# Performance work log

Hardware: AMD Instinct MI355X
Metric: run time of the kernel (lower is better)

## Reference

```python
import math
import jax, jax.numpy as jnp
import numpy as np

N_HEADS = 16
D_KV = 64
NUM_BUCKETS = 32
MAX_DISTANCE = 128


def _relative_position_bucket(relative_position, num_buckets=NUM_BUCKETS, max_distance=MAX_DISTANCE):
    # bidirectional=True (encoder)
    num_buckets //= 2
    n = -relative_position
    ret = (n < 0).astype(jnp.int32) * num_buckets
    n = jnp.abs(n)
    max_exact = num_buckets // 2
    is_small = n < max_exact
    val_if_large = max_exact + (
        jnp.log(jnp.maximum(n, 1).astype(jnp.float32) / max_exact)
        / math.log(max_distance / max_exact)
        * (num_buckets - max_exact)
    ).astype(jnp.int32)
    val_if_large = jnp.minimum(val_if_large, num_buckets - 1)
    return ret + jnp.where(is_small, n, val_if_large)


def setup_inputs() -> dict:
    key = jax.random.key(0)
    ks = jax.random.split(key, 6)
    B, S, D = 2, 2048, 1024
    scale = 0.02  # keep pre-softmax logits in a sane range
    return {
        "x": jax.random.normal(ks[0], (B, S, D), dtype=jnp.float32),
        "Wq": jax.random.normal(ks[1], (D, N_HEADS * D_KV), dtype=jnp.float32) * scale,
        "Wk": jax.random.normal(ks[2], (D, N_HEADS * D_KV), dtype=jnp.float32) * scale,
        "Wv": jax.random.normal(ks[3], (D, N_HEADS * D_KV), dtype=jnp.float32) * scale,
        "Wo": jax.random.normal(ks[4], (N_HEADS * D_KV, D), dtype=jnp.float32) * scale,
        "rel_emb": jax.random.normal(ks[5], (NUM_BUCKETS, N_HEADS), dtype=jnp.float32) * scale,
    }


def reference(x, Wq, Wk, Wv, Wo, rel_emb):
    B, S, D = x.shape
    H, Dk = N_HEADS, D_KV

    def shape(t):  # [B,S,H*Dk] -> [B,H,S,Dk]
        return t.reshape(B, S, H, Dk).transpose(0, 2, 1, 3)

    q = shape(x @ Wq)
    k = shape(x @ Wk)
    v = shape(x @ Wv)

    # NOTE: T5 attention has NO 1/sqrt(d) scaling.
    scores = jnp.einsum("bhqd,bhkd->bhqk", q, k)

    # relative position bias: [1, H, S, S]
    ctx_pos = jnp.arange(S)[:, None]
    mem_pos = jnp.arange(S)[None, :]
    rp_bucket = _relative_position_bucket(mem_pos - ctx_pos)  # [S, S]
    position_bias = rel_emb[rp_bucket].transpose(2, 0, 1)[None]  # [1,H,S,S]

    weights = jax.nn.softmax(scores + position_bias, axis=-1)
    context = jnp.einsum("bhqk,bhkd->bhqd", weights, v)
    context = context.transpose(0, 2, 1, 3).reshape(B, S, H * Dk)
    return context @ Wo
```

## Files before the change

kernel.cpp:

```cpp
#include <hip/hip_runtime.h>
#include <math.h>

typedef unsigned short u16;
typedef unsigned int u32;
typedef __attribute__((ext_vector_type(8))) short bf16x8_t;
typedef __attribute__((ext_vector_type(4))) float f32x4_t;

#define S_LEN  2048
#define NH     16
#define DK     64
#define DMODEL 1024
#define MROWS  4096

__device__ inline u16 f2b(float f) {
  union { float f; u32 u; } c; c.f = f;
  u32 u = c.u;
  return (u16)((u + 0x7fffu + ((u >> 16) & 1u)) >> 16);
}

__global__ void prep_kernel(const float* __restrict__ x,
                            const float* __restrict__ Wq, const float* __restrict__ Wk,
                            const float* __restrict__ Wv, const float* __restrict__ Wo,
                            const float* __restrict__ rel,
                            u16* __restrict__ xb, u16* __restrict__ Wall,
                            u16* __restrict__ Wto, float* __restrict__ btab) {
  __shared__ float tile[32][33];
  const int bid = blockIdx.x, t = threadIdx.x;
  if (bid < 4096) {
    int i = (bid * 256 + t) * 4;
    float4 v = *(const float4*)(x + i);
    ushort4 o;
    o.x = f2b(v.x); o.y = f2b(v.y); o.z = f2b(v.z); o.w = f2b(v.w);
    *(ushort4*)(xb + i) = o;
  } else if (bid < 8192) {
    int bid2 = bid - 4096;
    int z = bid2 >> 10, rem = bid2 & 1023;
    const float* W; u16* Wt;
    switch (z) {
      case 0: W = Wq; Wt = Wall; break;
      case 1: W = Wk; Wt = Wall + (size_t)DMODEL * DMODEL; break;
      case 2: W = Wv; Wt = Wall + (size_t)2 * DMODEL * DMODEL; break;
      default: W = Wo; Wt = Wto; break;
    }
    int bc = (rem & 31) * 32, br = (rem >> 5) * 32;
    int tx = t & 31, ty = t >> 5;
    #pragma unroll
    for (int yy = 0; yy < 32; yy += 8)
      tile[ty + yy][tx] = W[(size_t)(br + ty + yy) * DMODEL + bc + tx];
    __syncthreads();
    #pragma unroll
    for (int yy = 0; yy < 32; yy += 8)
      Wt[(size_t)(bc + ty + yy) * DMODEL + br + tx] = f2b(tile[tx][ty + yy]);
  } else {
    int idx = (bid - 8192) * 256 + t;
    if (idx < NH * 4095) {
      int h = idx / 4095;
      int dpos = idx - h * 4095;
      int delta = dpos - 2047;
      int ret = (delta > 0) ? 16 : 0;
      int n = delta < 0 ? -delta : delta;
      int bucket;
      if (n < 8) {
        bucket = ret + n;
      } else {
        float vf = logf((float)n * 0.125f) / 2.7725887222397811f * 8.0f;
        int vil = 8 + (int)vf;
        bucket = ret + (vil < 15 ? vil : 15);
      }
      btab[idx] = rel[bucket * NH + h] - 16.0f;
    }
  }
}

#define GSTR 56
__global__ __launch_bounds__(256) void gemm128_kernel(const u16* __restrict__ A,
                                                      const u16* __restrict__ Bt,
                                                      float* __restrict__ C,
                                                      u16* __restrict__ q16,
                                                      u16* __restrict__ k16,
                                                      u16* __restrict__ vt16,
                                                      int mode) {
  __shared__ __align__(16) u16 As[128 * GSTR];
  __shared__ __align__(16) u16 Bs[128 * GSTR];
  const int t = threadIdx.x, w = t >> 6, l = t & 63;
  const int c = l & 15, quad = l >> 4;
  const int m0 = blockIdx.x * 128, n0 = blockIdx.y * 128;
  const int wm = (w & 1) * 64, wn = (w >> 1) * 64;

  const int sr = t >> 2;
  const int k8 = (t & 3) * 8;
  const u16* Ag0 = A  + (size_t)(m0 + sr) * DMODEL + k8;
  const u16* Ag1 = Ag0 + (size_t)64 * DMODEL;
  const u16* Bg0 = Bt + (size_t)(n0 + sr) * DMODEL + k8;
  const u16* Bg1 = Bg0 + (size_t)64 * DMODEL;
  u16* Al0 = As + sr * GSTR + k8;
  u16* Al1 = Al0 + 64 * GSTR;
  u16* Bl0 = Bs + sr * GSTR + k8;
  u16* Bl1 = Bl0 + 64 * GSTR;

  uint4 a0 = *(const uint4*)Ag0, a1 = *(const uint4*)Ag1;
  uint4 b0 = *(const uint4*)Bg0, b1 = *(const uint4*)Bg1;

  f32x4_t acc[16] = {};
  for (int k0 = 0; k0 < DMODEL; k0 += 32) {
    __syncthreads();
    *(uint4*)Al0 = a0; *(uint4*)Al1 = a1;
    *(uint4*)Bl0 = b0; *(uint4*)Bl1 = b1;
    __syncthreads();
    if (k0 + 32 < DMODEL) {
      a0 = *(const uint4*)(Ag0 + k0 + 32);
      a1 = *(const uint4*)(Ag1 + k0 + 32);
      b0 = *(const uint4*)(Bg0 + k0 + 32);
      b1 = *(const uint4*)(Bg1 + k0 + 32);
    }
    bf16x8_t af[4], bfr[4];
    #pragma unroll
    for (int i = 0; i < 4; ++i) {
      af[i]  = *(const bf16x8_t*)(As + (wm + i * 16 + c) * GSTR + quad * 8);
      bfr[i] = *(const bf16x8_t*)(Bs + (wn + i * 16 + c) * GSTR + quad * 8);
    }
    #pragma unroll
    for (int mt = 0; mt < 4; ++mt)
      #pragma unroll
      for (int nt = 0; nt < 4; ++nt)
        acc[mt * 4 + nt] = __builtin_amdgcn_mfma_f32_16x16x32_bf16(af[mt], bfr[nt], acc[mt * 4 + nt], 0, 0, 0);
  }

  const int whichblk = n0 >> 10;
  if (mode == 0) {
    #pragma unroll
    for (int mt = 0; mt < 4; ++mt) {
      int grow0 = m0 + wm + mt * 16 + quad * 4;
      #pragma unroll
      for (int nt = 0; nt < 4; ++nt) {
        int gcol = n0 + wn + nt * 16 + c;
        #pragma unroll
        for (int r = 0; r < 4; ++r)
          C[(size_t)(grow0 + r) * DMODEL + gcol] = acc[mt * 4 + nt][r];
      }
    }
  } else if (whichblk == 2) {
    #pragma unroll
    for (int mt = 0; mt < 4; ++mt) {
      int grow0 = m0 + wm + mt * 16 + quad * 4;
      int b = grow0 >> 11, s0 = grow0 & 2047;
      #pragma unroll
      for (int nt = 0; nt < 4; ++nt) {
        int cc = (n0 + wn + nt * 16 + c) & 1023;
        int hh = cc >> 6, dk = cc & 63;
        f32x4_t v4 = acc[mt * 4 + nt];
        ushort4 o;
        o.x = f2b(v4[0]); o.y = f2b(v4[1]); o.z = f2b(v4[2]); o.w = f2b(v4[3]);
        *(ushort4*)(vt16 + (((size_t)(b * NH + hh)) * DK + dk) * S_LEN + s0) = o;
      }
    }
  } else {
    u16* tb = (w & 1) ? Bs : As;
    const int base_mw = m0 + wm;
    const int bb = base_mw >> 11, s0g = base_mw & 2047;
    const int cc = (n0 + wn) & 1023;
    const int hh = cc >> 6;
    u16* qk = (whichblk == 0 ? q16 : k16) + (((size_t)(bb * NH + hh)) * S_LEN + s0g) * DK;
    __syncthreads();
    #pragma unroll
    for (int round = 0; round < 2; ++round) {
      if ((w >> 1) == round) {
        #pragma unroll
        for (int mt = 0; mt < 4; ++mt)
          #pragma unroll
          for (int nt = 0; nt < 4; ++nt)
            #pragma unroll
            for (int r = 0; r < 4; ++r)
              tb[(mt * 16 + quad * 4 + r) * 72 + nt * 16 + c] = f2b(acc[mt * 4 + nt][r]);
        #pragma unroll
        for (int i = 0; i < 8; ++i) {
          int lrow = i * 8 + (l >> 3);
          int chk = l & 7;
          uint4 vv = *(const uint4*)(tb + lrow * 72 + chk * 8);
          *(uint4*)(qk + (size_t)lrow * DK + chk * 8) = vv;
        }
      }
      __syncthreads();
    }
  }
}

#define ASTR 72
__global__ __launch_bounds__(256, 4) void attn_mfma_kernel(const u16* __restrict__ q,
                                                           const u16* __restrict__ k,
                                                           const u16* __restrict__ vt,
                                                           const float* __restrict__ btab,
                                                           u16* __restrict__ ctx) {
  __shared__ __align__(16) u16 Ks[64 * ASTR];
  __shared__ __align__(16) u16 Vts[64 * ASTR];
  __shared__ __align__(16) u16 Ps[4 * 16 * ASTR];
  __shared__ float band[128];

  const int t = threadIdx.x;
  const int w = t >> 6, l = t & 63;
  const int c = l & 15, quad = l >> 4;
  const int bh = blockIdx.y;
  const int h = bh & (NH - 1), b = bh >> 4;
  const int q0 = blockIdx.x * 64;

  const u16* qb = q + (size_t)bh * S_LEN * DK;
  const u16* kb = k + (size_t)bh * S_LEN * DK;
  const u16* vb = vt + (size_t)bh * DK * S_LEN;
  const float* btp = btab + h * 4095 + (2047 - 63 - q0);

  bf16x8_t qfrag[2];
  {
    const u16* qp = qb + (size_t)(q0 + w * 16 + c) * DK + quad * 8;
    qfrag[0] = *(const bf16x8_t*)(qp);
    qfrag[1] = *(const bf16x8_t*)(qp + 32);
  }

  float lp[4] = {0.f, 0.f, 0.f, 0.f};
  f32x4_t O[4] = {};

  const int srow = t >> 3;
  const int sc8 = (t & 7) * 8;
  const u16* kg0 = kb + (size_t)srow * DK + sc8;
  const u16* kg1 = kg0 + (size_t)32 * DK;
  const u16* vg0 = vb + (size_t)srow * S_LEN + sc8;
  const u16* vg1 = vg0 + (size_t)32 * S_LEN;
  u16* Kl0 = Ks + srow * ASTR + sc8;
  u16* Kl1 = Kl0 + 32 * ASTR;
  u16* Vl0 = Vts + srow * ASTR + sc8;
  u16* Vl1 = Vl0 + 32 * ASTR;
  u16* Pw = Ps + w * 16 * ASTR;
  const int bnd0 = c - (w * 16 + quad * 4) + 63;

  uint4 kr0 = *(const uint4*)kg0, kr1 = *(const uint4*)kg1;
  uint4 vr0 = *(const uint4*)vg0, vr1 = *(const uint4*)vg1;
  float br = (t < 127) ? btp[t] : 0.f;

  for (int kt = 0; kt < S_LEN; kt += 64) {
    const int D = kt - q0;
    const bool far = (D >= 192) || (D <= -192);
    *(uint4*)Kl0 = kr0; *(uint4*)Kl1 = kr1;
    *(uint4*)Vl0 = vr0; *(uint4*)Vl1 = vr1;
    if (t < 127) band[t] = br;
    __syncthreads();
    if (kt + 64 < S_LEN) {
      kr0 = *(const uint4*)(kg0 + (size_t)(kt + 64) * DK);
      kr1 = *(const uint4*)(kg1 + (size_t)(kt + 64) * DK);
      vr0 = *(const uint4*)(vg0 + (kt + 64));
      vr1 = *(const uint4*)(vg1 + (kt + 64));
      br = (t < 127) ? btp[kt + 64 + t] : 0.f;
    }

    f32x4_t s4[4] = {};
    #pragma unroll
    for (int kc = 0; kc < 2; ++kc) {
      #pragma unroll
      for (int nt = 0; nt < 4; ++nt) {
        bf16x8_t bfr = *(const bf16x8_t*)(Ks + (nt * 16 + c) * ASTR + kc * 32 + quad * 8);
        s4[nt] = __builtin_amdgcn_mfma_f32_16x16x32_bf16(qfrag[kc], bfr, s4[nt], 0, 0, 0);
      }
    }

    if (far) {
      const float bf = btp[kt + 63];
      #pragma unroll
      for (int nt = 0; nt < 4; ++nt) {
        #pragma unroll
        for (int r = 0; r < 4; ++r) {
          float p = __expf(s4[nt][r] + bf);
          lp[r] += p;
          union { float f; u32 u; } cv; cv.f = p;
          Pw[(quad * 4 + r) * ASTR + nt * 16 + c] = (u16)((cv.u + 0x8000u) >> 16);
        }
      }
    } else {
      #pragma unroll
      for (int nt = 0; nt < 4; ++nt) {
        #pragma unroll
        for (int r = 0; r < 4; ++r) {
          float p = __expf(s4[nt][r] + band[bnd0 + nt * 16 - r]);
          lp[r] += p;
          union { float f; u32 u; } cv; cv.f = p;
          Pw[(quad * 4 + r) * ASTR + nt * 16 + c] = (u16)((cv.u + 0x8000u) >> 16);
        }
      }
    }

    #pragma unroll
    for (int kc = 0; kc < 2; ++kc) {
      bf16x8_t afr = *(const bf16x8_t*)(Pw + c * ASTR + kc * 32 + quad * 8);
      #pragma unroll
      for (int nt = 0; nt < 4; ++nt) {
        bf16x8_t bfr = *(const bf16x8_t*)(Vts + (nt * 16 + c) * ASTR + kc * 32 + quad * 8);
        O[nt] = __builtin_amdgcn_mfma_f32_16x16x32_bf16(afr, bfr, O[nt], 0, 0, 0);
      }
    }
    __syncthreads();
  }

  #pragma unroll
  for (int off = 1; off < 16; off <<= 1)
    #pragma unroll
    for (int r = 0; r < 4; ++r)
      lp[r] += __shfl_xor(lp[r], off, 64);
  #pragma unroll
  for (int r = 0; r < 4; ++r) {
    float inv = 1.0f / lp[r];
    int s = q0 + w * 16 + quad * 4 + r;
    u16* cp = ctx + ((size_t)(b * S_LEN + s)) * DMODEL + h * DK + c;
    #pragma unroll
    for (int nt = 0; nt < 4; ++nt)
      cp[nt * 16] = f2b(O[nt][r] * inv);
  }
}

extern "C" void kernel_launch(void* const* d_in, const int* in_sizes, int n_in,
                              void* d_out, int out_size, void* d_ws, size_t ws_size,
                              hipStream_t stream) {
  const float* x   = (const float*)d_in[0];
  const float* Wq  = (const float*)d_in[1];
  const float* Wk  = (const float*)d_in[2];
  const float* Wv  = (const float*)d_in[3];
  const float* Wo  = (const float*)d_in[4];
  const float* rel = (const float*)d_in[5];
  float* out = (float*)d_out;

  char* ws = (char*)d_ws;
  size_t off = 0;
  auto carve = [&](size_t bytes) -> char* {
    char* p = ws + off;
    off += (bytes + 255) & ~(size_t)255;
    return p;
  };
  u16*   xb   = (u16*)  carve((size_t)MROWS * DMODEL * 2);
  u16*   Wall = (u16*)  carve((size_t)3 * DMODEL * DMODEL * 2);
  u16*   Wto  = (u16*)  carve((size_t)DMODEL * DMODEL * 2);
  u16*   qb16 = (u16*)  carve((size_t)4194304 * 2);
  u16*   kb16 = (u16*)  carve((size_t)4194304 * 2);
  u16*   vt16 = (u16*)  carve((size_t)4194304 * 2);
  float* btab = (float*)carve(((size_t)NH * 4095 + 256) * 4);
  u16*   ctxb = (u16*)  carve((size_t)4194304 * 2);

  prep_kernel<<<8448, 256, 0, stream>>>(x, Wq, Wk, Wv, Wo, rel, xb, Wall, Wto, btab);

  dim3 qkvgrid(32, 24);
  gemm128_kernel<<<qkvgrid, 256, 0, stream>>>(xb, Wall, nullptr, qb16, kb16, vt16, 1);

  dim3 agrid(S_LEN / 64, 32);
  attn_mfma_kernel<<<agrid, 256, 0, stream>>>(qb16, kb16, vt16, btab, ctxb);

  dim3 ogrid(32, 8);
  gemm128_kernel<<<ogrid, 256, 0, stream>>>(ctxb, Wto, out, nullptr, nullptr, nullptr, 0);
}
```

Before: 216.8 us.

## Process 128 queries per attention block and use exp2 with prescaled bias

The attention kernel now handles 128 query rows per block, with each wave covering two 16-row groups. K and V fragments are loaded into registers once per tile and reused for both groups, which halves K/V global and LDS traffic per query. The bias table is prescaled by log2(e) so the softmax exponent becomes one fma followed by a hardware exp2. The grid shrinks to 512 blocks and register use per thread grows (the occupancy hint of 4 was dropped), so latency hiding may suffer.

```diff
diff --git a/kernel.cpp b/kernel.cpp
--- a/kernel.cpp
+++ b/kernel.cpp
@@ -11,11 +11,20 @@
 #define DK     64
 #define DMODEL 1024
 #define MROWS  4096
+#define LOG2E  1.44269504088896f
 
 __device__ inline u16 f2b(float f) {
   union { float f; u32 u; } c; c.f = f;
   u32 u = c.u;
   return (u16)((u + 0x7fffu + ((u >> 16) & 1u)) >> 16);
+}
+
+__device__ __forceinline__ float fexp2(float x) {
+#if __has_builtin(__builtin_amdgcn_exp2f)
+  return __builtin_amdgcn_exp2f(x);
+#else
+  return exp2f(x);
+#endif
 }
 
 __global__ void prep_kernel(const float* __restrict__ x,
@@ -67,7 +76,7 @@
         int vil = 8 + (int)vf;
         bucket = ret + (vil < 15 ? vil : 15);
       }
-      btab[idx] = rel[bucket * NH + h] - 16.0f;
+      btab[idx] = (rel[bucket * NH + h] - 16.0f) * LOG2E;
     }
   }
 }
@@ -186,37 +195,38 @@
 }
 
 #define ASTR 72
-__global__ __launch_bounds__(256, 4) void attn_mfma_kernel(const u16* __restrict__ q,
-                                                           const u16* __restrict__ k,
-                                                           const u16* __restrict__ vt,
-                                                           const float* __restrict__ btab,
-                                                           u16* __restrict__ ctx) {
+__global__ __launch_bounds__(256) void attn_mfma_kernel(const u16* __restrict__ q,
+                                                        const u16* __restrict__ k,
+                                                        const u16* __restrict__ vt,
+                                                        const float* __restrict__ btab,
+                                                        u16* __restrict__ ctx) {
   __shared__ __align__(16) u16 Ks[64 * ASTR];
   __shared__ __align__(16) u16 Vts[64 * ASTR];
-  __shared__ __align__(16) u16 Ps[4 * 16 * ASTR];
-  __shared__ float band[128];
+  __shared__ __align__(16) u16 Ps[4][16 * ASTR];
+  __shared__ float band[192];
 
   const int t = threadIdx.x;
   const int w = t >> 6, l = t & 63;
   const int c = l & 15, quad = l >> 4;
   const int bh = blockIdx.y;
   const int h = bh & (NH - 1), b = bh >> 4;
-  const int q0 = blockIdx.x * 64;
+  const int q0 = blockIdx.x * 128;
 
   const u16* qb = q + (size_t)bh * S_LEN * DK;
   const u16* kb = k + (size_t)bh * S_LEN * DK;
   const u16* vb = vt + (size_t)bh * DK * S_LEN;
-  const float* btp = btab + h * 4095 + (2047 - 63 - q0);
-
-  bf16x8_t qfrag[2];
-  {
-    const u16* qp = qb + (size_t)(q0 + w * 16 + c) * DK + quad * 8;
-    qfrag[0] = *(const bf16x8_t*)(qp);
-    qfrag[1] = *(const bf16x8_t*)(qp + 32);
-  }
-
-  float lp[4] = {0.f, 0.f, 0.f, 0.f};
-  f32x4_t O[4] = {};
+  const float* btp = btab + h * 4095 + (2047 - 127 - q0);
+
+  bf16x8_t qfrag[2][2];
+  #pragma unroll
+  for (int qg = 0; qg < 2; ++qg) {
+    const u16* qp = qb + (size_t)(q0 + w * 32 + qg * 16 + c) * DK + quad * 8;
+    qfrag[qg][0] = *(const bf16x8_t*)(qp);
+    qfrag[qg][1] = *(const bf16x8_t*)(qp + 32);
+  }
+
+  float lp[2][4] = {};
+  f32x4_t O[2][4] = {};
 
   const int srow = t >> 3;
   const int sc8 = (t & 7) * 8;
@@ -228,70 +238,81 @@
   u16* Kl1 = Kl0 + 32 * ASTR;
   u16* Vl0 = Vts + srow * ASTR + sc8;
   u16* Vl1 = Vl0 + 32 * ASTR;
-  u16* Pw = Ps + w * 16 * ASTR;
-  const int bnd0 = c - (w * 16 + quad * 4) + 63;
+  u16* Pw = Ps[w];
 
   uint4 kr0 = *(const uint4*)kg0, kr1 = *(const uint4*)kg1;
   uint4 vr0 = *(const uint4*)vg0, vr1 = *(const uint4*)vg1;
-  float br = (t < 127) ? btp[t] : 0.f;
+  float br = (t < 192) ? btp[t] : 0.f;
 
   for (int kt = 0; kt < S_LEN; kt += 64) {
     const int D = kt - q0;
-    const bool far = (D >= 192) || (D <= -192);
+    const bool far = (D >= 256) || (D <= -192);
     *(uint4*)Kl0 = kr0; *(uint4*)Kl1 = kr1;
     *(uint4*)Vl0 = vr0; *(uint4*)Vl1 = vr1;
-    if (t < 127) band[t] = br;
+    if (t < 192) band[t] = br;
     __syncthreads();
     if (kt + 64 < S_LEN) {
       kr0 = *(const uint4*)(kg0 + (size_t)(kt + 64) * DK);
       kr1 = *(const uint4*)(kg1 + (size_t)(kt + 64) * DK);
       vr0 = *(const uint4*)(vg0 + (kt + 64));
       vr1 = *(const uint4*)(vg1 + (kt + 64));
-      br = (t < 127) ? btp[kt + 64 + t] : 0.f;
-    }
-
-    f32x4_t s4[4] = {};
-    #pragma unroll
-    for (int kc = 0; kc < 2; ++kc) {
-      #pragma unroll
-      for (int nt = 0; nt < 4; ++nt) {
-        bf16x8_t bfr = *(const bf16x8_t*)(Ks + (nt * 16 + c) * ASTR + kc * 32 + quad * 8);
-        s4[nt] = __builtin_amdgcn_mfma_f32_16x16x32_bf16(qfrag[kc], bfr, s4[nt], 0, 0, 0);
-      }
-    }
-
-    if (far) {
-      const float bf = btp[kt + 63];
-      #pragma unroll
-      for (int nt = 0; nt < 4; ++nt) {
-        #pragma unroll
-        for (int r = 0; r < 4; ++r) {
-          float p = __expf(s4[nt][r] + bf);
-          lp[r] += p;
-          union { float f; u32 u; } cv; cv.f = p;
-          Pw[(quad * 4 + r) * ASTR + nt * 16 + c] = (u16)((cv.u + 0x8000u) >> 16);
-        }
-      }
-    } else {
-      #pragma unroll
-      for (int nt = 0; nt < 4; ++nt) {
-        #pragma unroll
-        for (int r = 0; r < 4; ++r) {
-          float p = __expf(s4[nt][r] + band[bnd0 + nt * 16 - r]);
-          lp[r] += p;
-          union { float f; u32 u; } cv; cv.f = p;
-          Pw[(quad * 4 + r) * ASTR + nt * 16 + c] = (u16)((cv.u + 0x8000u) >> 16);
-        }
-      }
-    }
-
-    #pragma unroll
-    for (int kc = 0; kc < 2; ++kc) {
-      bf16x8_t afr = *(const bf16x8_t*)(Pw + c * ASTR + kc * 32 + quad * 8);
-      #pragma unroll
-      for (int nt = 0; nt < 4; ++nt) {
-        bf16x8_t bfr = *(const bf16x8_t*)(Vts + (nt * 16 + c) * ASTR + kc * 32 + quad * 8);
-        O[nt] = __builtin_amdgcn_mfma_f32_16x16x32_bf16(afr, bfr, O[nt], 0, 0, 0);
+      br = (t < 192) ? btp[kt + 64 + t] : 0.f;
+    }
+
+    bf16x8_t kf[2][4];
+    #pragma unroll
+    for (int kc = 0; kc < 2; ++kc)
+      #pragma unroll
+      for (int nt = 0; nt < 4; ++nt)
+        kf[kc][nt] = *(const bf16x8_t*)(Ks + (nt * 16 + c) * ASTR + kc * 32 + quad * 8);
+
+    f32x4_t s4[2][4] = {};
+    #pragma unroll
+    for (int qg = 0; qg < 2; ++qg)
+      #pragma unroll
+      for (int kc = 0; kc < 2; ++kc)
+        #pragma unroll
+        for (int nt = 0; nt < 4; ++nt)
+          s4[qg][nt] = __builtin_amdgcn_mfma_f32_16x16x32_bf16(qfrag[qg][kc], kf[kc][nt], s4[qg][nt], 0, 0, 0);
+
+    bf16x8_t vf[2][4];
+    #pragma unroll
+    for (int kc = 0; kc < 2; ++kc)
+      #pragma unroll
+      for (int nt = 0; nt < 4; ++nt)
+        vf[kc][nt] = *(const bf16x8_t*)(Vts + (nt * 16 + c) * ASTR + kc * 32 + quad * 8);
+
+    const float bfc = band[127];
+    #pragma unroll
+    for (int qg = 0; qg < 2; ++qg) {
+      const int bnd0 = c - (w * 32 + qg * 16 + quad * 4) + 127;
+      if (far) {
+        #pragma unroll
+        for (int nt = 0; nt < 4; ++nt)
+          #pragma unroll
+          for (int r = 0; r < 4; ++r) {
+            float p = fexp2(fmaf(s4[qg][nt][r], LOG2E, bfc));
+            lp[qg][r] += p;
+            union { float f; u32 u; } cv; cv.f = p;
+            Pw[(quad * 4 + r) * ASTR + nt * 16 + c] = (u16)((cv.u + 0x8000u) >> 16);
+          }
+      } else {
+        #pragma unroll
+        for (int nt = 0; nt < 4; ++nt)
+          #pragma unroll
+          for (int r = 0; r < 4; ++r) {
+            float p = fexp2(fmaf(s4[qg][nt][r], LOG2E, band[bnd0 + nt * 16 - r]));
+            lp[qg][r] += p;
+            union { float f; u32 u; } cv; cv.f = p;
+            Pw[(quad * 4 + r) * ASTR + nt * 16 + c] = (u16)((cv.u + 0x8000u) >> 16);
+          }
+      }
+      #pragma unroll
+      for (int kc = 0; kc < 2; ++kc) {
+        bf16x8_t afr = *(const bf16x8_t*)(Pw + c * ASTR + kc * 32 + quad * 8);
+        #pragma unroll
+        for (int nt = 0; nt < 4; ++nt)
+          O[qg][nt] = __builtin_amdgcn_mfma_f32_16x16x32_bf16(afr, vf[kc][nt], O[qg][nt], 0, 0, 0);
       }
     }
     __syncthreads();
@@ -300,17 +321,21 @@
   #pragma unroll
   for (int off = 1; off < 16; off <<= 1)
     #pragma unroll
-    for (int r = 0; r < 4; ++r)
-      lp[r] += __shfl_xor(lp[r], off, 64);
+    for (int qg = 0; qg < 2; ++qg)
+      #pragma unroll
+      for (int r = 0; r < 4; ++r)
+        lp[qg][r] += __shfl_xor(lp[qg][r], off, 64);
   #pragma unroll
-  for (int r = 0; r < 4; ++r) {
-    float inv = 1.0f / lp[r];
-    int s = q0 + w * 16 + quad * 4 + r;
-    u16* cp = ctx + ((size_t)(b * S_LEN + s)) * DMODEL + h * DK + c;
-    #pragma unroll
-    for (int nt = 0; nt < 4; ++nt)
-      cp[nt * 16] = f2b(O[nt][r] * inv);
-  }
+  for (int qg = 0; qg < 2; ++qg)
+    #pragma unroll
+    for (int r = 0; r < 4; ++r) {
+      float inv = 1.0f / lp[qg][r];
+      int s = q0 + w * 32 + qg * 16 + quad * 4 + r;
+      u16* cp = ctx + ((size_t)(b * S_LEN + s)) * DMODEL + h * DK + c;
+      #pragma unroll
+      for (int nt = 0; nt < 4; ++nt)
+        cp[nt * 16] = f2b(O[qg][nt][r] * inv);
+    }
 }
 
 extern "C" void kernel_launch(void* const* d_in, const int* in_sizes, int n_in,
@@ -345,7 +370,7 @@
   dim3 qkvgrid(32, 24);
   gemm128_kernel<<<qkvgrid, 256, 0, stream>>>(xb, Wall, nullptr, qb16, kb16, vt16, 1);
 
-  dim3 agrid(S_LEN / 64, 32);
+  dim3 agrid(S_LEN / 128, 32);
   attn_mfma_kernel<<<agrid, 256, 0, stream>>>(qb16, kb16, vt16, btab, ctxb);
 
   dim3 ogrid(32, 8);
```

Result: faster. 208.6 us (-3.8%).
